# Kernel optimization log

Hardware: AMD Instinct MI355X
Metric: run time of the kernel (lower is better)

Reference implementation:

```python
import jax, jax.numpy as jnp
from jax import lax
import numpy as np

LEVELS = 17
VAR_N = 4
UNITS = 3 * LEVELS          # 51 neurons: motor 17, command 13, inter 21
MOTOR = LEVELS
PRED_N = 4
UNFOLDS = 6                 # ncps LTC default ode_unfolds
EPS = 1e-8
B = 32768                   # recurrence length = B + PRED_N
D = VAR_N * LEVELS          # 68


def _build_wiring(seed=0):
    # AutoNCP(51, 17, sparsity_level=0.8): inter=21, command=13, motor=17
    # sensory_fanout=4, inter_fanout=2, 5 recurrent command synapses, motor_fanin=2
    rng = np.random.default_rng(seed)
    motor, command, S = 17, 13, LEVELS
    N = UNITS
    cmd = np.arange(motor, motor + command)
    intr = np.arange(motor + command, N)
    adj = np.zeros((N, N), np.float32)
    sadj = np.zeros((S, N), np.float32)
    pol = lambda: float(rng.choice([-1.0, 1.0]))
    for s in range(S):
        for d in rng.choice(intr, 4, replace=False):
            sadj[s, d] = pol()
    for d in intr:
        if not sadj[:, d].any():
            sadj[int(rng.integers(S)), d] = pol()
    for i in intr:
        for d in rng.choice(cmd, 2, replace=False):
            adj[i, d] = pol()
    for d in cmd:
        if not adj[intr, d].any():
            adj[int(rng.choice(intr)), d] = pol()
    for _ in range(5):
        adj[int(rng.choice(cmd)), int(rng.choice(cmd))] = pol()
    for m in range(motor):
        for srci in rng.choice(cmd, 2, replace=False):
            adj[srci, m] = pol()
    return adj, sadj


def setup_inputs():
    key = jax.random.key(0)
    ks = iter(jax.random.split(key, 48))
    u = lambda s, lo, hi: jax.random.uniform(next(ks), s, jnp.float32, lo, hi)
    lin = lambda i, o: jax.random.normal(next(ks), (i, o), jnp.float32) * (i ** -0.5)
    adj, sadj = _build_wiring()
    V, N, S = VAR_N, UNITS, LEVELS
    M1 = (LEVELS + D) // 2           # 42
    G = VAR_N * D                    # 272
    G2 = (G + D) // 2                # 170
    return dict(
        x=jax.random.normal(next(ks), (B, D), jnp.float32),
        pre_w1=lin(D, D), pre_b1=jnp.zeros((D,), jnp.float32),
        pre_w2=lin(D, D), pre_b2=jnp.zeros((D,), jnp.float32),
        gleak=u((V, N), 0.001, 1.0), vleak=u((V, N), -0.2, 0.2), cm=u((V, N), 0.4, 0.6),
        w=u((V, N, N), 0.001, 1.0), sigma=u((V, N, N), 3.0, 8.0), mu=u((V, N, N), 0.3, 0.8),
        erev=jnp.asarray(np.tile(adj, (V, 1, 1))),
        sens_w=u((V, S, N), 0.001, 1.0), sens_sigma=u((V, S, N), 3.0, 8.0), sens_mu=u((V, S, N), 0.3, 0.8),
        sens_erev=jnp.asarray(np.tile(sadj, (V, 1, 1))),
        in_w=jnp.ones((V, S), jnp.float32), in_b=jnp.zeros((V, S), jnp.float32),
        out_w=jnp.ones((V, MOTOR), jnp.float32), out_b=jnp.zeros((V, MOTOR), jnp.float32),
        tW1=lin(LEVELS, LEVELS), tb1=jnp.zeros((LEVELS,), jnp.float32),
        tW2=lin(LEVELS, M1), tb2=jnp.zeros((M1,), jnp.float32),
        tW3=lin(M1, D), tb3=jnp.zeros((D,), jnp.float32),
        gW1=lin(G, G), gb1=jnp.zeros((G,), jnp.float32),
        gW2=lin(G, G2), gb2=jnp.zeros((G2,), jnp.float32),
        gW3=lin(G2, D), gb3=jnp.zeros((D,), jnp.float32),
        mask=jnp.asarray((adj != 0).astype(np.float32)),
        sens_mask=jnp.asarray((sadj != 0).astype(np.float32)),
    )


def _forward(x, pre_w1, pre_b1, pre_w2, pre_b2,
             gleak, vleak, cm, w, sigma, mu, erev,
             sens_w, sens_sigma, sens_mu, sens_erev,
             in_w, in_b, out_w, out_b,
             tW1, tb1, tW2, tb2, tW3, tb3,
             gW1, gb1, gW2, gb2, gW3, gb3,
             mask, sens_mask, ckpt=False):
    sig = jax.nn.sigmoid
    # VarEncoder: Linear -> Sigmoid -> Linear
    h = sig(x @ pre_w1 + pre_b1) @ pre_w2 + pre_b2                  # (B, 68)
    xs = h.reshape(-1, VAR_N, LEVELS).transpose(1, 0, 2)            # (V, B, 17)
    seqs = jnp.concatenate([xs, jnp.repeat(xs[:, -1:, :], PRED_N, axis=1)], axis=1)  # (V, T, 17)

    def run(p, seq):
        gl_, vl_, cm_, w_, sg_, mu_, er_, sw_, ssg_, smu_, ser_, iw_, ib_, ow_, ob_ = p
        gl = jax.nn.softplus(gl_)                 # (N,)
        wp = jax.nn.softplus(w_) * mask           # (N, N) sparse NCP wiring
        swp = jax.nn.softplus(sw_) * sens_mask    # (S, N)
        cmt = jax.nn.softplus(cm_) * UNFOLDS      # cm / (elapsed=1 / unfolds)

        def step(v, u_in):
            u = u_in * iw_ + ib_                                   # affine input mapping
            sact = swp * sig((u[:, None] - smu_) * ssg_)           # (S, N)
            num_s = (sact * ser_).sum(0)
            den_s = sact.sum(0)

            def unfold(vv, _):
                wa = wp * sig((vv[:, None] - mu_) * sg_)           # (N, N), src axis 0
                vv = (cmt * vv + gl * vl_ + (wa * er_).sum(0) + num_s) / (
                    cmt + gl + wa.sum(0) + den_s + EPS)
                return vv, None

            v, _ = lax.scan(unfold, v, None, length=UNFOLDS)
            return v, v[:MOTOR] * ow_ + ob_                        # affine output mapping

        stepf = jax.checkpoint(step) if ckpt else step
        _, outs = lax.scan(stepf, jnp.zeros((UNITS,), seq.dtype), seq)
        return outs                                                # (T, 17)

    p = (gleak, vleak, cm, w, sigma, mu, erev,
         sens_w, sens_sigma, sens_mu, sens_erev, in_w, in_b, out_w, out_b)
    rs = jax.vmap(run, in_axes=(0, 0))(p, seqs)                    # (V, T, 17)
    r = rs.transpose(1, 0, 2)                                      # (T, V, 17)
    # CrossConnector: per-tile MLP 17->17->42->68 (sigmoids), flatten, 272->272->170->68
    t = sig(sig(sig(r @ tW1 + tb1) @ tW2 + tb2) @ tW3 + tb3)        # (T, V, 68)
    g = t.reshape(t.shape[0], -1)                                   # (T, 272)
    return sig(sig(g @ gW1 + gb1) @ gW2 + gb2) @ gW3 + gb3          # (T, 68)


def reference(x, pre_w1, pre_b1, pre_w2, pre_b2,
              gleak, vleak, cm, w, sigma, mu, erev,
              sens_w, sens_sigma, sens_mu, sens_erev,
              in_w, in_b, out_w, out_b,
              tW1, tb1, tW2, tb2, tW3, tb3,
              gW1, gb1, gW2, gb2, gW3, gb3,
              mask, sens_mask):
    return _forward(x, pre_w1, pre_b1, pre_w2, pre_b2,
                    gleak, vleak, cm, w, sigma, mu, erev,
                    sens_w, sens_sigma, sens_mu, sens_erev,
                    in_w, in_b, out_w, out_b,
                    tW1, tb1, tW2, tb2, tW3, tb3,
                    gW1, gb1, gW2, gb2, gW3, gb3,
                    mask, sens_mask)
```

## Files before the change

### kernel.cpp

```cpp
#include <hip/hip_runtime.h>
#include <hip/hip_bf16.h>
#include <math.h>

#define LEVELS 17
#define VARN   4
#define UNITS  51
#define MOTOR  17
#define NB     32768
#define TT     (NB + 4)
#define DD     68
#define LOG2E  1.4426950408889634f
#define TROWS  16

#define W_WARM  10
#define L_CHUNK 18
#define NCHUNK  ((TT + L_CHUNK - 1) / L_CHUNK)

#define W_F     64
#define L_F     64
#define NCHUNK_F ((TT + L_F - 1) / L_F)
#define CAP_R  16

#define MROWS  48
#define MBLK   ((TT + MROWS - 1) / MROWS)
#define EBLK   ((NB + MROWS - 1) / MROWS)
#define BUFSZ  (48 * 272 + 64)
#define EBUFSZ (48 * 72 + 64)

#define OFF_WA 0
#define OFF_WB 7680
#define OFF_WC 24576
#define OFF_WD 76800
#define OFF_WE 155136
#define OFF_WF 205824
#define OFF_P1 221184
#define OFF_P2 228864
#define WTS_SHORTS 236544
#define PSENS_N (VARN * LEVELS * UNITS)

typedef __attribute__((ext_vector_type(8))) short short8v;
typedef __attribute__((ext_vector_type(4))) float f32x4;

__device__ __forceinline__ float fast_rcp(float x) { return __builtin_amdgcn_rcpf(x); }
__device__ __forceinline__ float fast_exp2(float x) { return __builtin_amdgcn_exp2f(x); }
__device__ __forceinline__ float sigf(float x) { return fast_rcp(1.0f + __expf(-x)); }
__device__ __forceinline__ float softplusf(float x) { return logf(1.0f + expf(x)); }
__device__ __forceinline__ unsigned short f2bf(float x) {
    unsigned int u = __float_as_uint(x);
    unsigned int r = u + 0x7FFFu + ((u >> 16) & 1u);
    return (unsigned short)(r >> 16);
}

__global__ __launch_bounds__(256) void prep_weights(
    const float* __restrict__ tW1, const float* __restrict__ tW2, const float* __restrict__ tW3,
    const float* __restrict__ gW1, const float* __restrict__ gW2, const float* __restrict__ gW3,
    const float* __restrict__ pW1, const float* __restrict__ pW2,
    unsigned short* __restrict__ wts)
{
    const int ph = blockIdx.y;
    const int KTt[8]   = {3, 3, 6, 9, 9, 6, 3, 3};
    const int NCt[8]   = {5, 11, 17, 17, 11, 5, 5, 5};
    const int offsT[8] = {OFF_WA, OFF_WB, OFF_WC, OFF_WD, OFF_WE, OFF_WF, OFF_P1, OFF_P2};
    int S = NCt[ph] * KTt[ph] * 512;
    int idx = blockIdx.x * 256 + threadIdx.x;
    if (idx >= S) return;
    int tile = idx >> 9;
    int r    = idx & 511;
    int lane = r >> 3;
    int e    = r & 7;
    int KTp  = KTt[ph];
    int ct   = tile / KTp;
    int kt   = tile - ct * KTp;
    int n = ct * 16 + (lane & 15);
    int k = kt * 32 + (lane >> 4) * 8 + e;
    float val = 0.0f;
    switch (ph) {
        case 0: if (k < 68 && n < 68) { int v = k / 17; if (n / 17 == v) val = tW1[(k % 17) * 17 + (n % 17)]; } break;
        case 1: if (k < 68 && n < 168) { int v = k / 17; int c = n - 42 * v; if (c >= 0 && c < 42) val = tW2[(k % 17) * 42 + c]; } break;
        case 2: if (k < 168 && n < 272) { int v = k / 42; int c = n - 68 * v; if (c >= 0 && c < 68) val = tW3[(k % 42) * 68 + c]; } break;
        case 3: if (k < 272 && n < 272) val = gW1[k * 272 + n]; break;
        case 4: if (k < 272 && n < 170) val = gW2[k * 170 + n]; break;
        case 5: if (k < 170 && n < 68)  val = gW3[k * 68 + n]; break;
        case 6: if (k < 68 && n < 68)   val = pW1[k * 68 + n]; break;
        case 7: if (k < 68 && n < 68)   val = pW2[k * 68 + n]; break;
    }
    wts[offsT[ph] + idx] = f2bf(val);
}

__global__ __launch_bounds__(256) void prep_sens(
    const float* __restrict__ sens_w, const float* __restrict__ sens_sigma,
    const float* __restrict__ sens_mu, const float* __restrict__ sens_erev,
    float4* __restrict__ psens)
{
    int idx = blockIdx.x * 256 + threadIdx.x;
    if (idx >= PSENS_N) return;
    float sg = sens_sigma[idx], m = sens_mu[idx];
    float wf = softplusf(sens_w[idx]);
    psens[idx] = make_float4(fast_exp2(sg * m * LOG2E), -sg * LOG2E, wf, wf * sens_erev[idx]);
}

template<int KT, int NC>
__device__ __forceinline__ void mfma_phase(
    const unsigned short* __restrict__ wt,
    const unsigned short* __restrict__ bufIn, int ldkIn,
    unsigned short* __restrict__ bufOut, int ldkOut,
    const float* __restrict__ bias, int bmod, int Nvalid,
    int lane, int wave)
{
    #pragma unroll
    for (int rt = 0; rt < 3; ++rt) {
        short8v af[KT];
        int abase = (rt * 16 + (lane & 15)) * ldkIn + 8 * (lane >> 4);
        #pragma unroll
        for (int kt = 0; kt < KT; ++kt)
            af[kt] = *reinterpret_cast<const short8v*>(&bufIn[abase + kt * 32]);
        for (int ct = wave; ct < NC; ct += 4) {
            int c = ct * 16 + (lane & 15);
            const unsigned short* wp = wt + (size_t)(ct * KT) * 512 + lane * 8;
            short8v bf[KT];
            #pragma unroll
            for (int kt = 0; kt < KT; ++kt)
                bf[kt] = *reinterpret_cast<const short8v*>(&wp[kt * 512]);
            f32x4 acc = {0.0f, 0.0f, 0.0f, 0.0f};
            #pragma unroll
            for (int kt = 0; kt < KT; ++kt)
                acc = __builtin_amdgcn_mfma_f32_16x16x32_bf16(af[kt], bf[kt], acc, 0, 0, 0);
            float bv = 0.0f;
            if (c < Nvalid) {
                int cb = (bmod == 0) ? (c % 17) : (bmod == 1) ? (c % 42) : (bmod == 2) ? (c % 68) : c;
                bv = bias[cb];
            }
            #pragma unroll
            for (int i = 0; i < 4; ++i) {
                float vv = sigf(acc[i] + bv);
                int rl = rt * 16 + (lane >> 4) * 4 + i;
                if (c < ldkOut) bufOut[rl * ldkOut + c] = f2bf(vv);
            }
        }
    }
}

template<int KT>
__device__ __forceinline__ void mfma_final(
    const unsigned short* __restrict__ wt,
    const unsigned short* __restrict__ bufIn, int ldkIn,
    float* __restrict__ io, int baseRow,
    const float* __restrict__ gb3, int lane, int wave)
{
    #pragma unroll
    for (int rt = 0; rt < 3; ++rt) {
        short8v af[KT];
        int abase = (rt * 16 + (lane & 15)) * ldkIn + 8 * (lane >> 4);
        #pragma unroll
        for (int kt = 0; kt < KT; ++kt)
            af[kt] = *reinterpret_cast<const short8v*>(&bufIn[abase + kt * 32]);
        for (int ct = wave; ct < 5; ct += 4) {
            int c = ct * 16 + (lane & 15);
            const unsigned short* wp = wt + (size_t)(ct * KT) * 512 + lane * 8;
            short8v bf[KT];
            #pragma unroll
            for (int kt = 0; kt < KT; ++kt)
                bf[kt] = *reinterpret_cast<const short8v*>(&wp[kt * 512]);
            f32x4 acc = {0.0f, 0.0f, 0.0f, 0.0f};
            #pragma unroll
            for (int kt = 0; kt < KT; ++kt)
                acc = __builtin_amdgcn_mfma_f32_16x16x32_bf16(af[kt], bf[kt], acc, 0, 0, 0);
            float bv = (c < 68) ? gb3[c] : 0.0f;
            #pragma unroll
            for (int i = 0; i < 4; ++i) {
                int row = baseRow + rt * 16 + (lane >> 4) * 4 + i;
                if (c < 68 && row < TT) io[(size_t)row * DD + c] = acc[i] + bv;
            }
        }
    }
}

__global__ __launch_bounds__(256) void mlp_mfma(
    float* __restrict__ io, const unsigned short* __restrict__ wts,
    const float* __restrict__ tb1, const float* __restrict__ tb2, const float* __restrict__ tb3,
    const float* __restrict__ gb1, const float* __restrict__ gb2, const float* __restrict__ gb3)
{
    __shared__ unsigned short buf0[BUFSZ];
    __shared__ unsigned short buf1[BUFSZ];
    int tid = threadIdx.x, lane = tid & 63, wave = tid >> 6;
    int baseRow = blockIdx.x * MROWS;

    for (int e = tid; e < BUFSZ; e += 256) { buf0[e] = 0; buf1[e] = 0; }
    __syncthreads();
    for (int e = tid; e < MROWS * DD; e += 256) {
        int r = e / DD, c = e % DD;
        int gr = baseRow + r;
        float xv = (gr < TT) ? io[(size_t)gr * DD + c] : 0.0f;
        buf0[r * 72 + c] = f2bf(xv);
    }
    __syncthreads();
    mfma_phase<3, 5 >(wts + OFF_WA, buf0, 72,  buf1, 72,  tb1, 0, 68,  lane, wave); __syncthreads();
    mfma_phase<3, 11>(wts + OFF_WB, buf1, 72,  buf0, 168, tb2, 1, 168, lane, wave); __syncthreads();
    mfma_phase<6, 17>(wts + OFF_WC, buf0, 168, buf1, 272, tb3, 2, 272, lane, wave); __syncthreads();
    mfma_phase<9, 17>(wts + OFF_WD, buf1, 272, buf0, 272, gb1, 3, 272, lane, wave); __syncthreads();
    mfma_phase<9, 11>(wts + OFF_WE, buf0, 272, buf1, 176, gb2, 3, 170, lane, wave); __syncthreads();
    mfma_final<6>(wts + OFF_WF, buf1, 176, io, baseRow, gb3, lane, wave);
}

__global__ __launch_bounds__(256) void enc_mfma(
    const float* __restrict__ x, const unsigned short* __restrict__ wts,
    const float* __restrict__ pb1, const float* __restrict__ pb2,
    float* __restrict__ seq)
{
    __shared__ unsigned short buf0[EBUFSZ];
    __shared__ unsigned short buf1[EBUFSZ];
    int tid = threadIdx.x, lane = tid & 63, wave = tid >> 6;
    int baseRow = blockIdx.x * MROWS;

    for (int e = tid; e < EBUFSZ; e += 256) { buf0[e] = 0; buf1[e] = 0; }
    __syncthreads();
    for (int e = tid; e < MROWS * DD; e += 256) {
        int r = e / DD, c = e % DD;
        int gr = baseRow + r;
        float xv = (gr < NB) ? x[(size_t)gr * DD + c] : 0.0f;
        buf0[r * 72 + c] = f2bf(xv);
    }
    __syncthreads();
    mfma_phase<3, 5>(wts + OFF_P1, buf0, 72, buf1, 72, pb1, 3, 68, lane, wave);
    __syncthreads();
    #pragma unroll
    for (int rt = 0; rt < 3; ++rt) {
        short8v af[3];
        int abase = (rt * 16 + (lane & 15)) * 72 + 8 * (lane >> 4);
        #pragma unroll
        for (int kt = 0; kt < 3; ++kt)
            af[kt] = *reinterpret_cast<const short8v*>(&buf1[abase + kt * 32]);
        for (int ct = wave; ct < 5; ct += 4) {
            int c = ct * 16 + (lane & 15);
            const unsigned short* wp = wts + OFF_P2 + (size_t)(ct * 3) * 512 + lane * 8;
            short8v bf[3];
            #pragma unroll
            for (int kt = 0; kt < 3; ++kt)
                bf[kt] = *reinterpret_cast<const short8v*>(&wp[kt * 512]);
            f32x4 acc = {0.0f, 0.0f, 0.0f, 0.0f};
            #pragma unroll
            for (int kt = 0; kt < 3; ++kt)
                acc = __builtin_amdgcn_mfma_f32_16x16x32_bf16(af[kt], bf[kt], acc, 0, 0, 0);
            float bv = (c < 68) ? pb2[c] : 0.0f;
            #pragma unroll
            for (int i = 0; i < 4; ++i) {
                int row = baseRow + rt * 16 + (lane >> 4) * 4 + i;
                if (c < 68 && row < NB) {
                    float vv = acc[i] + bv;
                    int v = c / 17, s = c % 17;
                    float* dst = seq + ((size_t)v * TT + row) * LEVELS + s;
                    dst[0] = vv;
                    if (row == NB - 1) {
                        dst[1 * LEVELS] = vv; dst[2 * LEVELS] = vv;
                        dst[3 * LEVELS] = vv; dst[4 * LEVELS] = vv;
                    }
                }
            }
        }
    }
}

__global__ __launch_bounds__(256) void sens_kernel(
    const float* __restrict__ seq,
    const float4* __restrict__ psens,
    const float* __restrict__ in_w, const float* __restrict__ in_b,
    const float* __restrict__ sens_mask,
    float2* __restrict__ tab)
{
    __shared__ float us_sh[4][LEVELS];
    int grp = threadIdx.x >> 6;
    int j   = threadIdx.x & 63;
    int tt  = blockIdx.x * 4 + grp;
    int v   = blockIdx.y;
    bool live = (tt < TT);
    if (live && j < LEVELS) {
        float xv = seq[((size_t)v * TT + tt) * LEVELS + j];
        us_sh[grp][j] = fmaf(xv, in_w[v * LEVELS + j], in_b[v * LEVELS + j]);
    }
    __syncthreads();
    if (!live || j >= UNITS) return;
    unsigned int bits = 0;
    for (int s = 0; s < LEVELS; ++s)
        bits |= (sens_mask[s * UNITS + j] != 0.0f ? 1u : 0u) << s;
    float num = 0.0f, den = 0.0f;
    while (bits) {
        int s = __ffs(bits) - 1; bits &= bits - 1;
        float4 p = psens[(v * LEVELS + s) * UNITS + j];
        float g = fast_rcp(fmaf(p.x, fast_exp2(p.y * us_sh[grp][s]), 1.0f));
        num = fmaf(p.w, g, num);
        den = fmaf(p.z, g, den);
    }
    tab[((size_t)v * TT + tt) * UNITS + j] = make_float2(num, den);
}

template<int MH>
__device__ void scan_body(
    int j, int jn, bool hasHelp, int partner, int myStart, int myCnt,
    unsigned long long colbits, int v, int t0, int wstart, int tend,
    float cmt, float glvl, float cgl, float ow, float ob, bool isHelper,
    const float* __restrict__ w, const float* __restrict__ sigma,
    const float* __restrict__ mu, const float* __restrict__ erev,
    const float2* __restrict__ tab, float* __restrict__ rout)
{
    int   src[MH]; float fw[MH], fc[MH], fk[MH], fwfe[MH];
    unsigned long long bits = colbits;
    for (int s = 0; s < myStart; ++s) bits &= bits - 1;
    #pragma unroll
    for (int k = 0; k < MH; ++k) {
        bool on = (k < myCnt);
        int sc = on ? (__ffsll((unsigned long long)bits) - 1) : 0;
        src[k] = sc;
        size_t pi = ((size_t)v * UNITS + sc) * UNITS + jn;
        float sg = on ? sigma[pi] : 0.0f;
        float m  = on ? mu[pi]    : 0.0f;
        fw[k] = on ? softplusf(w[pi]) : 0.0f;
        fc[k] = fast_exp2(sg * m * LOG2E);
        fk[k] = -sg * LOG2E;
        fwfe[k] = on ? fw[k] * erev[pi] : 0.0f;
        if (on) bits &= bits - 1;
    }
    const float2* tp = tab + (size_t)v * TT * UNITS + jn;
    float* rp = rout + (size_t)v * LEVELS + j;
    float2 nd = tp[(size_t)t0 * UNITS];
    float vreg = 0.0f;
    for (int t = t0; t < tend; ++t) {
        float2 ndc = nd;
        if (t + 1 < tend) nd = tp[(size_t)(t + 1) * UNITS];
        float bn = isHelper ? 0.0f : (glvl + ndc.x);
        float bd = isHelper ? 0.0f : (cgl + ndc.y);
        #pragma unroll
        for (int uf = 0; uf < 6; ++uf) {
            float vs[MH];
            #pragma unroll
            for (int k = 0; k < MH; ++k) vs[k] = __shfl(vreg, src[k], 64);
            float num = bn, den = bd;
            #pragma unroll
            for (int k = 0; k < MH; ++k) {
                float g = fast_rcp(fmaf(fc[k], fast_exp2(fk[k] * vs[k]), 1.0f));
                num = fmaf(fwfe[k], g, num);
                den = fmaf(fw[k], g, den);
            }
            float pn = __shfl(num, partner, 64);
            float pd = __shfl(den, partner, 64);
            if (hasHelp) { num += pn; den += pd; }
            vreg = fmaf(cmt, vreg, num) * fast_rcp(den);
        }
        if (j < MOTOR && t >= wstart) rp[(size_t)t * DD] = fmaf(vreg, ow, ob);
    }
}

__device__ void scan_body_gen(
    int j, int jn, bool hasHelp, int partner, int myStart, int myCnt, int mcMax,
    unsigned long long colbits, int v, int t0, int wstart, int tend,
    float cmt, float glvl, float cgl, float ow, float ob, bool isHelper,
    const float* __restrict__ w, const float* __restrict__ sigma,
    const float* __restrict__ mu, const float* __restrict__ erev,
    const float2* __restrict__ tab, float* __restrict__ rout)
{
    unsigned long long mybits = colbits;
    for (int s = 0; s < myStart; ++s) mybits &= mybits - 1;
    const float2* tp = tab + (size_t)v * TT * UNITS + jn;
    float* rp = rout + (size_t)v * LEVELS + j;
    float vreg = 0.0f;
    for (int t = t0; t < tend; ++t) {
        float2 ndc = tp[(size_t)t * UNITS];
        float bn = isHelper ? 0.0f : (glvl + ndc.x);
        float bd = isHelper ? 0.0f : (cgl + ndc.y);
        for (int uf = 0; uf < 6; ++uf) {
            unsigned long long bits = mybits;
            float num = bn, den = bd;
            for (int k = 0; k < mcMax; ++k) {
                bool on = (k < myCnt) && (bits != 0ull);
                int sc = on ? (__ffsll(bits) - 1) : 0;
                if (on) bits &= bits - 1;
                float vs = __shfl(vreg, sc, 64);
                size_t pi = ((size_t)v * UNITS + sc) * UNITS + jn;
                float a = on ? softplusf(w[pi]) * sigf((vs - mu[pi]) * sigma[pi]) : 0.0f;
                num = fmaf(a, on ? erev[pi] : 0.0f, num);
                den += a;
            }
            float pn = __shfl(num, partner, 64);
            float pd = __shfl(den, partner, 64);
            if (hasHelp) { num += pn; den += pd; }
            vreg = fmaf(cmt, vreg, num) * fast_rcp(den);
        }
        if (j < MOTOR && t >= wstart) rp[(size_t)t * DD] = fmaf(vreg, ow, ob);
    }
}

__global__ __launch_bounds__(256, 8) void scan_pre(
    const float2* __restrict__ tab,
    const float* __restrict__ gleak, const float* __restrict__ vleak, const float* __restrict__ cm,
    const float* __restrict__ w, const float* __restrict__ sigma,
    const float* __restrict__ mu, const float* __restrict__ erev,
    const float* __restrict__ out_w, const float* __restrict__ out_b,
    const float* __restrict__ mask,
    float* __restrict__ rout)
{
    int gwi = (blockIdx.x << 2) + (threadIdx.x >> 6);
    int j = threadIdx.x & 63;
    int v = gwi & 3;
    int chunk = gwi >> 2;
    if (chunk >= NCHUNK) return;
    int wstart = chunk * L_CHUNK;
    int tend = min(TT, wstart + L_CHUNK);
    int t0 = max(0, wstart - W_WARM);

    bool isHelper = (j >= UNITS);
    int jn = isHelper ? (j - 34) : j;
    unsigned long long colbits = 0ull;
    for (int i = 0; i < UNITS; ++i)
        colbits |= (unsigned long long)(mask[i * UNITS + jn] != 0.0f ? 1 : 0) << i;
    int nf = __popcll(colbits);
    bool isCmd = (jn >= MOTOR && jn < MOTOR + 13);
    int nh = (nf + 1) >> 1;
    int myStart, myCnt;
    if (isHelper)    { myStart = nh; myCnt = nf - nh; }
    else if (isCmd)  { myStart = 0;  myCnt = nh; }
    else             { myStart = 0;  myCnt = nf; }
    bool hasHelp = (!isHelper) && isCmd;
    int partner = hasHelp ? (jn + 34) : j;

    float cmt  = softplusf(cm[v * UNITS + jn]) * 6.0f;
    float gl   = softplusf(gleak[v * UNITS + jn]);
    float glvl = gl * vleak[v * UNITS + jn];
    float cgl  = cmt + gl + 1e-8f;
    float ow = (j < MOTOR) ? out_w[v * LEVELS + j] : 0.0f;
    float ob = (j < MOTOR) ? out_b[v * LEVELS + j] : 0.0f;

    int mc = myCnt;
    #pragma unroll
    for (int off = 32; off; off >>= 1) mc = max(mc, __shfl_xor(mc, off, 64));

    if (mc <= 4)
        scan_body<4>(j, jn, hasHelp, partner, myStart, myCnt, colbits, v, t0, wstart, tend,
                     cmt, glvl, cgl, ow, ob, isHelper, w, sigma, mu, erev, tab, rout);
    else if (mc <= 6)
        scan_body<6>(j, jn, hasHelp, partner, myStart, myCnt, colbits, v, t0, wstart, tend,
                     cmt, glvl, cgl, ow, ob, isHelper, w, sigma, mu, erev, tab, rout);
    else if (mc <= 8)
        scan_body<8>(j, jn, hasHelp, partner, myStart, myCnt, colbits, v, t0, wstart, tend,
                     cmt, glvl, cgl, ow, ob, isHelper, w, sigma, mu, erev, tab, rout);
    else
        scan_body_gen(j, jn, hasHelp, partner, myStart, myCnt, mc, colbits, v, t0, wstart, tend,
                      cmt, glvl, cgl, ow, ob, isHelper, w, sigma, mu, erev, tab, rout);
}

__global__ __launch_bounds__(128) void enc_kernel(
    const float* __restrict__ x,
    const float* __restrict__ W1, const float* __restrict__ b1,
    const float* __restrict__ W2, const float* __restrict__ b2,
    float* __restrict__ seq)
{
    int t = blockIdx.x;
    int j = threadIdx.x;
    __shared__ float xs[DD];
    __shared__ float h1[DD];
    if (j < DD) xs[j] = x[(size_t)t * DD + j];
    __syncthreads();
    if (j < DD) {
        float acc = b1[j];
        #pragma unroll 4
        for (int k = 0; k < DD; ++k) acc = fmaf(xs[k], W1[k * DD + j], acc);
        h1[j] = sigf(acc);
    }
    __syncthreads();
    if (j < DD) {
        float acc = b2[j];
        #pragma unroll 4
        for (int k = 0; k < DD; ++k) acc = fmaf(h1[k], W2[k * DD + j], acc);
        int v = j / LEVELS, s = j % LEVELS;
        float* dst = seq + ((size_t)v * TT + t) * LEVELS + s;
        dst[0] = acc;
        if (t == NB - 1) {
            dst[1 * LEVELS] = acc; dst[2 * LEVELS] = acc;
            dst[3 * LEVELS] = acc; dst[4 * LEVELS] = acc;
        }
    }
}

template<int MF, int MS>
__device__ __forceinline__ void scan_loop_f(
    int j, int v, int t0, int wstart, int tend,
    const float* __restrict__ seq, float* __restrict__ rout,
    float cmt, float glvl, float cgl, float iw, float ib, float ow, float ob,
    int nf, int ns,
    const int* rs_, const float* rw_, const float* rc_, const float* rk_, const float* re_,
    const int* ss_, const float* sw_, const float* sc_, const float* sk_, const float* se_)
{
    int fs[MF]; float fw[MF], fc[MF], fk[MF], fe[MF];
    #pragma unroll
    for (int k = 0; k < MF; ++k) {
        bool on = k < nf;
        int idx = j * CAP_R + k;
        fs[k] = on ? rs_[idx] : 0;
        fw[k] = on ? rw_[idx] : 0.0f;
        fc[k] = on ? rc_[idx] : 1.0f;
        fk[k] = on ? rk_[idx] : 0.0f;
        fe[k] = on ? re_[idx] : 0.0f;
    }
    int gs[MS]; float gw[MS], gc[MS], gk[MS], ge[MS];
    #pragma unroll
    for (int k = 0; k < MS; ++k) {
        bool on = k < ns;
        int idx = j * LEVELS + k;
        gs[k] = on ? ss_[idx] : 0;
        gw[k] = on ? sw_[idx] : 0.0f;
        gc[k] = on ? sc_[idx] : 1.0f;
        gk[k] = on ? sk_[idx] : 0.0f;
        ge[k] = on ? se_[idx] : 0.0f;
    }
    const float* sp = seq + (size_t)v * TT * LEVELS + j;
    float* rp = rout + (size_t)v * LEVELS + j;
    float xnext = (j < LEVELS) ? sp[(size_t)t0 * LEVELS] : 0.0f;
    float vreg = 0.0f;
    for (int t = t0; t < tend; ++t) {
        float u = fmaf(xnext, iw, ib);
        if (j < LEVELS && t + 1 < tend) xnext = sp[(size_t)(t + 1) * LEVELS];
        float us[MS];
        #pragma unroll
        for (int k = 0; k < MS; ++k) us[k] = __shfl(u, gs[k], 64);
        float sa[MS];
        #pragma unroll
        for (int k = 0; k < MS; ++k)
            sa[k] = gw[k] * fast_rcp(fmaf(gc[k], fast_exp2(gk[k] * us[k]), 1.0f));
        float bn = glvl, bd = cgl;
        #pragma unroll
        for (int k = 0; k < MS; ++k) { bn = fmaf(sa[k], ge[k], bn); bd += sa[k]; }
        #pragma unroll
        for (int uf = 0; uf < 6; ++uf) {
            float vsa[MF];
            #pragma unroll
            for (int k = 0; k < MF; ++k) vsa[k] = __shfl(vreg, fs[k], 64);
            float aa[MF];
            #pragma unroll
            for (int k = 0; k < MF; ++k)
                aa[k] = fw[k] * fast_rcp(fmaf(fc[k], fast_exp2(fk[k] * vsa[k]), 1.0f));
            float num = bn, den = bd;
            #pragma unroll
            for (int k = 0; k < MF; ++k) { num = fmaf(aa[k], fe[k], num); den += aa[k]; }
            vreg = fmaf(cmt, vreg, num) * fast_rcp(den);
        }
        if (j < LEVELS && t >= wstart) rp[(size_t)t * DD] = fmaf(vreg, ow, ob);
    }
}

__global__ __launch_bounds__(64) void scan_fallback(
    const float* __restrict__ seq,
    const float* __restrict__ gleak, const float* __restrict__ vleak, const float* __restrict__ cm,
    const float* __restrict__ w, const float* __restrict__ sigma,
    const float* __restrict__ mu, const float* __restrict__ erev,
    const float* __restrict__ sens_w, const float* __restrict__ sens_sigma,
    const float* __restrict__ sens_mu, const float* __restrict__ sens_erev,
    const float* __restrict__ in_w, const float* __restrict__ in_b,
    const float* __restrict__ out_w, const float* __restrict__ out_b,
    const float* __restrict__ mask, const float* __restrict__ sens_mask,
    float* __restrict__ rout)
{
    __shared__ int   rs_[UNITS * CAP_R];
    __shared__ float rw_[UNITS * CAP_R], rc_[UNITS * CAP_R], rk_[UNITS * CAP_R], re_[UNITS * CAP_R];
    __shared__ int   ss_[UNITS * LEVELS];
    __shared__ float sw_[UNITS * LEVELS], sc_[UNITS * LEVELS], sk_[UNITS * LEVELS], se_[UNITS * LEVELS];
    __shared__ int   cnts[64], scnts[64];
    __shared__ int   red[2];

    int j = threadIdx.x;
    int v = blockIdx.x & 3;
    int chunk = blockIdx.x >> 2;
    int wstart = chunk * L_F;
    if (wstart >= TT) return;
    int tend = min(TT, wstart + L_F);
    int t0 = max(0, wstart - W_F);

    int nf = 0, ns = 0;
    if (j < UNITS) {
        for (int i = 0; i < UNITS; ++i) {
            if (mask[i * UNITS + j] != 0.0f) {
                if (nf < CAP_R) {
                    size_t pi = ((size_t)v * UNITS + i) * UNITS + j;
                    int idx = j * CAP_R + nf;
                    float sg = sigma[pi], m = mu[pi];
                    rs_[idx] = i;
                    rw_[idx] = softplusf(w[pi]);
                    rc_[idx] = fast_exp2(sg * m * LOG2E);
                    rk_[idx] = -sg * LOG2E;
                    re_[idx] = erev[pi];
                }
                nf++;
            }
        }
        for (int s = 0; s < LEVELS; ++s) {
            if (sens_mask[s * UNITS + j] != 0.0f) {
                size_t pi = ((size_t)v * LEVELS + s) * UNITS + j;
                int idx = j * LEVELS + ns;
                float sg = sens_sigma[pi], m = sens_mu[pi];
                ss_[idx] = s;
                sw_[idx] = softplusf(sens_w[pi]);
                sc_[idx] = fast_exp2(sg * m * LOG2E);
                sk_[idx] = -sg * LOG2E;
                se_[idx] = sens_erev[pi];
                ns++;
            }
        }
    }
    cnts[j] = nf; scnts[j] = ns;
    __syncthreads();
    if (j == 0) {
        int mf = 0, ms = 0;
        for (int i = 0; i < UNITS; ++i) { mf = max(mf, cnts[i]); ms = max(ms, scnts[i]); }
        red[0] = mf; red[1] = ms;
    }
    __syncthreads();
    int maxF = red[0], maxS = red[1];

    int jc = (j < UNITS) ? j : (UNITS - 1);
    float cmt  = softplusf(cm[v * UNITS + jc]) * 6.0f;
    float gl   = softplusf(gleak[v * UNITS + jc]);
    float glvl = gl * vleak[v * UNITS + jc];
    float cgl  = cmt + gl + 1e-8f;
    float iw = (j < LEVELS) ? in_w[v * LEVELS + j]  : 0.0f;
    float ib = (j < LEVELS) ? in_b[v * LEVELS + j]  : 0.0f;
    float ow = (j < LEVELS) ? out_w[v * LEVELS + j] : 0.0f;
    float ob = (j < LEVELS) ? out_b[v * LEVELS + j] : 0.0f;

    if (maxF <= 11 && maxS <= 12)
        scan_loop_f<11, 12>(j, v, t0, wstart, tend, seq, rout, cmt, glvl, cgl, iw, ib, ow, ob, nf, ns,
                            rs_, rw_, rc_, rk_, re_, ss_, sw_, sc_, sk_, se_);
    else
        scan_loop_f<16, 17>(j, v, t0, wstart, tend, seq, rout, cmt, glvl, cgl, iw, ib, ow, ob, nf, ns,
                            rs_, rw_, rc_, rk_, re_, ss_, sw_, sc_, sk_, se_);
}

__global__ __launch_bounds__(256) void mlp_kernel(
    float* __restrict__ io,
    const float* __restrict__ tW1, const float* __restrict__ tb1,
    const float* __restrict__ tW2, const float* __restrict__ tb2,
    const float* __restrict__ tW3, const float* __restrict__ tb3,
    const float* __restrict__ gW1, const float* __restrict__ gb1,
    const float* __restrict__ gW2, const float* __restrict__ gb2,
    const float* __restrict__ gW3, const float* __restrict__ gb3)
{
    __shared__ __align__(16) float A[TROWS][272];
    __shared__ __align__(16) float Bf[TROWS][272];
    int base = blockIdx.x * TROWS;
    int tid = threadIdx.x;

    for (int e = tid; e < TROWS * DD; e += 256) {
        int r = e / DD, c = e % DD;
        A[r][c] = (base + r < TT) ? io[(size_t)(base + r) * DD + c] : 0.0f;
    }
    __syncthreads();
    for (int c = tid; c < 4 * LEVELS; c += 256) {
        int vv = c / LEVELS, cc = c % LEVELS;
        float acc[TROWS]; float bias = tb1[cc];
        #pragma unroll
        for (int r = 0; r < TROWS; ++r) acc[r] = bias;
        for (int k = 0; k < LEVELS; ++k) {
            float wv = tW1[k * LEVELS + cc];
            #pragma unroll
            for (int r = 0; r < TROWS; ++r) acc[r] = fmaf(A[r][vv * LEVELS + k], wv, acc[r]);
        }
        #pragma unroll
        for (int r = 0; r < TROWS; ++r) Bf[r][c] = sigf(acc[r]);
    }
    __syncthreads();
    for (int c = tid; c < 4 * 42; c += 256) {
        int vv = c / 42, cc = c % 42;
        float acc[TROWS]; float bias = tb2[cc];
        #pragma unroll
        for (int r = 0; r < TROWS; ++r) acc[r] = bias;
        for (int k = 0; k < LEVELS; ++k) {
            float wv = tW2[k * 42 + cc];
            #pragma unroll
            for (int r = 0; r < TROWS; ++r) acc[r] = fmaf(Bf[r][vv * LEVELS + k], wv, acc[r]);
        }
        #pragma unroll
        for (int r = 0; r < TROWS; ++r) A[r][vv * 42 + cc] = sigf(acc[r]);
    }
    __syncthreads();
    for (int c = tid; c < 4 * DD; c += 256) {
        int vv = c / DD, cc = c % DD;
        float acc[TROWS]; float bias = tb3[cc];
        #pragma unroll
        for (int r = 0; r < TROWS; ++r) acc[r] = bias;
        for (int k = 0; k < 42; ++k) {
            float wv = tW3[k * DD + cc];
            #pragma unroll
            for (int r = 0; r < TROWS; ++r) acc[r] = fmaf(A[r][vv * 42 + k], wv, acc[r]);
        }
        #pragma unroll
        for (int r = 0; r < TROWS; ++r) Bf[r][c] = sigf(acc[r]);
    }
    __syncthreads();
    for (int c = tid; c < 272; c += 256) {
        float acc[TROWS]; float bias = gb1[c];
        #pragma unroll
        for (int r = 0; r < TROWS; ++r) acc[r] = bias;
        for (int k = 0; k < 272; k += 4) {
            float w0 = gW1[(k + 0) * 272 + c];
            float w1 = gW1[(k + 1) * 272 + c];
            float w2 = gW1[(k + 2) * 272 + c];
            float w3 = gW1[(k + 3) * 272 + c];
            #pragma unroll
            for (int r = 0; r < TROWS; ++r) {
                float4 g4 = *reinterpret_cast<const float4*>(&Bf[r][k]);
                acc[r] = fmaf(g4.x, w0, fmaf(g4.y, w1, fmaf(g4.z, w2, fmaf(g4.w, w3, acc[r]))));
            }
        }
        #pragma unroll
        for (int r = 0; r < TROWS; ++r) A[r][c] = sigf(acc[r]);
    }
    __syncthreads();
    for (int c = tid; c < 170; c += 256) {
        float acc[TROWS]; float bias = gb2[c];
        #pragma unroll
        for (int r = 0; r < TROWS; ++r) acc[r] = bias;
        for (int k = 0; k < 272; k += 4) {
            float w0 = gW2[(k + 0) * 170 + c];
            float w1 = gW2[(k + 1) * 170 + c];
            float w2 = gW2[(k + 2) * 170 + c];
            float w3 = gW2[(k + 3) * 170 + c];
            #pragma unroll
            for (int r = 0; r < TROWS; ++r) {
                float4 g4 = *reinterpret_cast<const float4*>(&A[r][k]);
                acc[r] = fmaf(g4.x, w0, fmaf(g4.y, w1, fmaf(g4.z, w2, fmaf(g4.w, w3, acc[r]))));
            }
        }
        #pragma unroll
        for (int r = 0; r < TROWS; ++r) Bf[r][c] = sigf(acc[r]);
    }
    __syncthreads();
    for (int c = tid; c < DD; c += 256) {
        float acc[TROWS]; float bias = gb3[c];
        #pragma unroll
        for (int r = 0; r < TROWS; ++r) acc[r] = bias;
        for (int k = 0; k < 168; k += 4) {
            float w0 = gW3[(k + 0) * DD + c];
            float w1 = gW3[(k + 1) * DD + c];
            float w2 = gW3[(k + 2) * DD + c];
            float w3 = gW3[(k + 3) * DD + c];
            #pragma unroll
            for (int r = 0; r < TROWS; ++r) {
                float4 g4 = *reinterpret_cast<const float4*>(&Bf[r][k]);
                acc[r] = fmaf(g4.x, w0, fmaf(g4.y, w1, fmaf(g4.z, w2, fmaf(g4.w, w3, acc[r]))));
            }
        }
        for (int k = 168; k < 170; ++k) {
            float wv = gW3[k * DD + c];
            #pragma unroll
            for (int r = 0; r < TROWS; ++r) acc[r] = fmaf(Bf[r][k], wv, acc[r]);
        }
        #pragma unroll
        for (int r = 0; r < TROWS; ++r)
            if (base + r < TT) io[(size_t)(base + r) * DD + c] = acc[r];
    }
}

extern "C" void kernel_launch(void* const* d_in, const int* in_sizes, int n_in,
                              void* d_out, int out_size, void* d_ws, size_t ws_size,
                              hipStream_t stream)
{
    (void)in_sizes; (void)n_in; (void)out_size;
    const float* x        = (const float*)d_in[0];
    const float* pre_w1   = (const float*)d_in[1];
    const float* pre_b1   = (const float*)d_in[2];
    const float* pre_w2   = (const float*)d_in[3];
    const float* pre_b2   = (const float*)d_in[4];
    const float* gleak    = (const float*)d_in[5];
    const float* vleak    = (const float*)d_in[6];
    const float* cm       = (const float*)d_in[7];
    const float* w        = (const float*)d_in[8];
    const float* sigma    = (const float*)d_in[9];
    const float* mu       = (const float*)d_in[10];
    const float* erev     = (const float*)d_in[11];
    const float* sens_w   = (const float*)d_in[12];
    const float* sens_sig = (const float*)d_in[13];
    const float* sens_mu  = (const float*)d_in[14];
    const float* sens_er  = (const float*)d_in[15];
    const float* in_w     = (const float*)d_in[16];
    const float* in_b     = (const float*)d_in[17];
    const float* out_w    = (const float*)d_in[18];
    const float* out_b    = (const float*)d_in[19];
    const float* tW1      = (const float*)d_in[20];
    const float* tb1      = (const float*)d_in[21];
    const float* tW2      = (const float*)d_in[22];
    const float* tb2      = (const float*)d_in[23];
    const float* tW3      = (const float*)d_in[24];
    const float* tb3      = (const float*)d_in[25];
    const float* gW1      = (const float*)d_in[26];
    const float* gb1      = (const float*)d_in[27];
    const float* gW2      = (const float*)d_in[28];
    const float* gb2      = (const float*)d_in[29];
    const float* gW3      = (const float*)d_in[30];
    const float* gb3      = (const float*)d_in[31];
    const float* mask     = (const float*)d_in[32];
    const float* smask    = (const float*)d_in[33];

    float* out = (float*)d_out;

    size_t tab_bytes = (size_t)VARN * TT * UNITS * sizeof(float2);
    size_t seq_bytes = (size_t)VARN * TT * LEVELS * sizeof(float);
    size_t wts_bytes = (size_t)WTS_SHORTS * sizeof(unsigned short);
    size_t ps_bytes  = (size_t)PSENS_N * sizeof(float4);

    if (ws_size >= tab_bytes + seq_bytes + wts_bytes + ps_bytes) {
        float2* tab = (float2*)d_ws;
        float*  seq = (float*)((char*)d_ws + tab_bytes);
        unsigned short* wts = (unsigned short*)((char*)d_ws + tab_bytes + seq_bytes);
        float4* psens = (float4*)((char*)d_ws + tab_bytes + seq_bytes + wts_bytes);
        prep_weights<<<dim3(306, 8), 256, 0, stream>>>(
            tW1, tW2, tW3, gW1, gW2, gW3, pre_w1, pre_w2, wts);
        prep_sens<<<(PSENS_N + 255) / 256, 256, 0, stream>>>(
            sens_w, sens_sig, sens_mu, sens_er, psens);
        enc_mfma<<<EBLK, 256, 0, stream>>>(x, wts, pre_b1, pre_b2, seq);
        sens_kernel<<<dim3((TT + 3) / 4, VARN), 256, 0, stream>>>(
            seq, psens, in_w, in_b, smask, tab);
        scan_pre<<<NCHUNK, 256, 0, stream>>>(
            tab, gleak, vleak, cm, w, sigma, mu, erev, out_w, out_b, mask, out);
        mlp_mfma<<<MBLK, 256, 0, stream>>>(out, wts, tb1, tb2, tb3, gb1, gb2, gb3);
    } else if (ws_size >= seq_bytes) {
        float* seq = (float*)d_ws;
        enc_kernel<<<NB, 128, 0, stream>>>(x, pre_w1, pre_b1, pre_w2, pre_b2, seq);
        scan_fallback<<<VARN * NCHUNK_F, 64, 0, stream>>>(
            seq, gleak, vleak, cm, w, sigma, mu, erev,
            sens_w, sens_sig, sens_mu, sens_er,
            in_w, in_b, out_w, out_b, mask, smask, out);
        mlp_kernel<<<(TT + TROWS - 1) / TROWS, 256, 0, stream>>>(
            out, tW1, tb1, tW2, tb2, tW3, tb3, gW1, gb1, gW2, gb2, gW3, gb3);
    }
}
```

Measured before the change: 278.2 us.

## Give each sens wave a slab of timesteps and enlarge scan chunk length

The sensory-table kernel now assigns one 64-lane wave to a 16-timestep slab for a single variable. The mask bits, input weights and loop bounds are computed once per slab and reused across steps. The shared-memory stage and block barrier are replaced by a wavefront shuffle of the scaled input. Separately, the scan chunk length goes from 18 to 34, which halves the number of chunks and so the warm-up overhead. In exchange there are fewer blocks for parallelism and more serial work per scan chunk.

```diff
diff --git a/kernel.cpp b/kernel.cpp
--- a/kernel.cpp
+++ b/kernel.cpp
@@ -13,7 +13,7 @@
 #define TROWS  16
 
 #define W_WARM  10
-#define L_CHUNK 18
+#define L_CHUNK 34
 #define NCHUNK  ((TT + L_CHUNK - 1) / L_CHUNK)
 
 #define W_F     64
@@ -260,6 +260,7 @@
     }
 }
 
+#define SENS_TPW 16
 __global__ __launch_bounds__(256) void sens_kernel(
     const float* __restrict__ seq,
     const float4* __restrict__ psens,
@@ -267,30 +268,42 @@
     const float* __restrict__ sens_mask,
     float2* __restrict__ tab)
 {
-    __shared__ float us_sh[4][LEVELS];
-    int grp = threadIdx.x >> 6;
+    int gwi = blockIdx.x * 4 + (threadIdx.x >> 6);
     int j   = threadIdx.x & 63;
-    int tt  = blockIdx.x * 4 + grp;
-    int v   = blockIdx.y;
-    bool live = (tt < TT);
-    if (live && j < LEVELS) {
-        float xv = seq[((size_t)v * TT + tt) * LEVELS + j];
-        us_sh[grp][j] = fmaf(xv, in_w[v * LEVELS + j], in_b[v * LEVELS + j]);
-    }
-    __syncthreads();
-    if (!live || j >= UNITS) return;
-    unsigned int bits = 0;
-    for (int s = 0; s < LEVELS; ++s)
-        bits |= (sens_mask[s * UNITS + j] != 0.0f ? 1u : 0u) << s;
-    float num = 0.0f, den = 0.0f;
-    while (bits) {
-        int s = __ffs(bits) - 1; bits &= bits - 1;
-        float4 p = psens[(v * LEVELS + s) * UNITS + j];
-        float g = fast_rcp(fmaf(p.x, fast_exp2(p.y * us_sh[grp][s]), 1.0f));
-        num = fmaf(p.w, g, num);
-        den = fmaf(p.z, g, den);
-    }
-    tab[((size_t)v * TT + tt) * UNITS + j] = make_float2(num, den);
+    int v    = gwi & 3;
+    int tbase = (gwi >> 2) * SENS_TPW;
+    if (tbase >= TT) return;
+
+    unsigned int bits0 = 0;
+    if (j < UNITS)
+        for (int s = 0; s < LEVELS; ++s)
+            bits0 |= (sens_mask[s * UNITS + j] != 0.0f ? 1u : 0u) << s;
+    int ns = __popc(bits0);
+    int mS = ns;
+    #pragma unroll
+    for (int off = 32; off; off >>= 1) mS = max(mS, __shfl_xor(mS, off, 64));
+
+    float iw = (j < LEVELS) ? in_w[v * LEVELS + j] : 0.0f;
+    float ib = (j < LEVELS) ? in_b[v * LEVELS + j] : 0.0f;
+
+    int tend = min(TT, tbase + SENS_TPW);
+    for (int t = tbase; t < tend; ++t) {
+        float u = (j < LEVELS)
+            ? fmaf(seq[((size_t)v * TT + t) * LEVELS + j], iw, ib) : 0.0f;
+        unsigned int bits = bits0;
+        float num = 0.0f, den = 0.0f;
+        for (int k = 0; k < mS; ++k) {
+            bool on = (k < ns) && (bits != 0u);
+            int s = on ? (__ffs(bits) - 1) : 0;
+            if (on) bits &= bits - 1;
+            float us = __shfl(u, s, 64);
+            float4 p = psens[(v * LEVELS + s) * UNITS + (j < UNITS ? j : 0)];
+            float g = fast_rcp(fmaf(p.x, fast_exp2(p.y * us), 1.0f));
+            if (on) { num = fmaf(p.w, g, num); den = fmaf(p.z, g, den); }
+        }
+        if (j < UNITS)
+            tab[((size_t)v * TT + t) * UNITS + j] = make_float2(num, den);
+    }
 }
 
 template<int MH>
@@ -813,8 +826,12 @@
         prep_sens<<<(PSENS_N + 255) / 256, 256, 0, stream>>>(
             sens_w, sens_sig, sens_mu, sens_er, psens);
         enc_mfma<<<EBLK, 256, 0, stream>>>(x, wts, pre_b1, pre_b2, seq);
-        sens_kernel<<<dim3((TT + 3) / 4, VARN), 256, 0, stream>>>(
-            seq, psens, in_w, in_b, smask, tab);
+        {
+            int slabs = (TT + SENS_TPW - 1) / SENS_TPW;
+            int waves = slabs * VARN;
+            sens_kernel<<<(waves + 3) / 4, 256, 0, stream>>>(
+                seq, psens, in_w, in_b, smask, tab);
+        }
         scan_pre<<<NCHUNK, 256, 0, stream>>>(
             tab, gleak, vleak, cm, w, sigma, mu, erev, out_w, out_b, mask, out);
         mlp_mfma<<<MBLK, 256, 0, stream>>>(out, wts, tb1, tb2, tb3, gb1, gb2, gb3);
```

Result: faster. 251.4 us (-9.6%).
